# Performance work log

Hardware: AMD Instinct MI355X
Metric: run time of the kernel (lower is better)

The kernel has to match this reference:

```python
import jax, jax.numpy as jnp
import numpy as np

N = 50000          # nodes
E = 800000         # edges (before self-loops)
IN = 128           # in_channels
C = 32             # hidden_channels
H = 4              # heads
SLOPE = 0.2        # PyG GATConv default negative_slope
NUM_CLASSES = 2


def setup_inputs() -> dict:
    key = jax.random.key(0)
    ks = jax.random.split(key, 20)
    s = 0.1
    inp = {
        "x": jax.random.normal(ks[0], (N, IN), jnp.float32),
        "edge_index": jax.random.randint(ks[1], (2, E), 0, N, jnp.int64),
        # conv1: IN -> H*C (concat)
        "W1": jax.random.normal(ks[2], (IN, H * C), jnp.float32) * s,
        "a1_src": jax.random.normal(ks[3], (H, C), jnp.float32) * s,
        "a1_dst": jax.random.normal(ks[4], (H, C), jnp.float32) * s,
        "b1": jnp.zeros((H * C,), jnp.float32),
        # conv2: H*C -> H*C (concat)
        "W2": jax.random.normal(ks[5], (H * C, H * C), jnp.float32) * s,
        "a2_src": jax.random.normal(ks[6], (H, C), jnp.float32) * s,
        "a2_dst": jax.random.normal(ks[7], (H, C), jnp.float32) * s,
        "b2": jnp.zeros((H * C,), jnp.float32),
        # conv3: H*C -> C (heads=1, concat=False)
        "W3": jax.random.normal(ks[8], (H * C, C), jnp.float32) * s,
        "a3_src": jax.random.normal(ks[9], (1, C), jnp.float32) * s,
        "a3_dst": jax.random.normal(ks[10], (1, C), jnp.float32) * s,
        "b3": jnp.zeros((C,), jnp.float32),
        # node classification head: C -> 2
        "Wc": jax.random.normal(ks[11], (C, NUM_CLASSES), jnp.float32) * s,
        "bc": jnp.zeros((NUM_CLASSES,), jnp.float32),
    }
    return inp


def gat_conv(x, src, dst, W, a_src, a_dst, b, heads, out_c, concat):
    """PyG-style GATConv with self-loops already appended to (src, dst)."""
    n = x.shape[0]
    h = (x @ W).reshape(n, heads, out_c)            # [N,H,C]
    al_src = jnp.sum(h * a_src, axis=-1)            # [N,H]
    al_dst = jnp.sum(h * a_dst, axis=-1)            # [N,H]
    e = al_src[src] + al_dst[dst]                   # [Et,H]
    e = jax.nn.leaky_relu(e, SLOPE)
    # numerically-stable segment softmax over edges sharing a destination
    emax = jax.ops.segment_max(e, dst, num_segments=n)   # every node has a self-loop
    e = jnp.exp(e - emax[dst])
    denom = jax.ops.segment_sum(e, dst, num_segments=n)
    alpha = e / (denom[dst] + 1e-16)                # [Et,H]
    msg = h[src] * alpha[:, :, None]                # [Et,H,C]
    out = jax.ops.segment_sum(msg, dst, num_segments=n)  # [N,H,C]
    out = out.reshape(n, heads * out_c) if concat else jnp.mean(out, axis=1)
    return out + b


def reference(x, edge_index, W1, a1_src, a1_dst, b1, W2, a2_src, a2_dst, b2,
              W3, a3_src, a3_dst, b3, Wc, bc):
    n = x.shape[0]
    loop = jnp.arange(n, dtype=edge_index.dtype)
    src = jnp.concatenate([edge_index[0], loop])
    dst = jnp.concatenate([edge_index[1], loop])
    h = jax.nn.elu(gat_conv(x, src, dst, W1, a1_src, a1_dst, b1, H, C, True))
    h = jax.nn.elu(gat_conv(h, src, dst, W2, a2_src, a2_dst, b2, H, C, True))
    h = gat_conv(h, src, dst, W3, a3_src, a3_dst, b3, 1, C, False)
    node_output = h @ Wc + bc                       # [N,2]
    link_embedding = h                              # [N,C]
    return (node_output, link_embedding)
```

## Files before the change

### kernel.cpp

```cpp
#include <hip/hip_runtime.h>
#include <math.h>

#define SLOPE 0.2f

__device__ __forceinline__ float lrelu(float x) { return x > 0.f ? x : SLOPE * x; }

__device__ __forceinline__ float bflo(unsigned int u) { return __uint_as_float(u << 16); }
__device__ __forceinline__ float bfhi(unsigned int u) { return __uint_as_float(u & 0xffff0000u); }
__device__ __forceinline__ unsigned short f2bf(float f) {
    unsigned int u = __float_as_uint(f);
    unsigned int r = u + 0x7fffu + ((u >> 16) & 1u);
    return (unsigned short)(r >> 16);
}

template <int COUT, int Hh, int NPT>
__global__ __launch_bounds__(256) void transform_kernel(
    const float* __restrict__ xin, const float* __restrict__ W,
    const float* __restrict__ a_src, const float* __restrict__ a_dst,
    unsigned short* __restrict__ hout, float* __restrict__ alsrc,
    float* __restrict__ aldst, int N)
{
    constexpr int JT = COUT / 4;
    constexpr int GROUPS = 256 / JT;
    constexpr int NB = GROUPS * NPT;
    constexpr int PAD = 4;
    __shared__ __align__(16) float xs[NB][128 + PAD];

    const int node0 = blockIdx.x * NB;
    const int total4 = NB * 32;
    const int lim4 = (N - node0) * 32;
    const float4* src4 = (const float4*)(xin + (size_t)node0 * 128);
    for (int i = threadIdx.x; i < total4; i += 256) {
        int row = i >> 5, col = i & 31;
        float4 v = (i < lim4) ? src4[i] : make_float4(0.f, 0.f, 0.f, 0.f);
        *(float4*)&xs[row][col << 2] = v;
    }
    __syncthreads();

    const int jt = threadIdx.x % JT;
    const int g  = threadIdx.x / JT;
    const int j4 = jt * 4;

    float4 acc[NPT];
#pragma unroll
    for (int m = 0; m < NPT; ++m) acc[m] = make_float4(0.f, 0.f, 0.f, 0.f);

    const float4* Wf4 = (const float4*)W;
    for (int k4 = 0; k4 < 32; ++k4) {
        float4 w0 = Wf4[(4 * k4 + 0) * JT + jt];
        float4 w1 = Wf4[(4 * k4 + 1) * JT + jt];
        float4 w2 = Wf4[(4 * k4 + 2) * JT + jt];
        float4 w3 = Wf4[(4 * k4 + 3) * JT + jt];
#pragma unroll
        for (int m = 0; m < NPT; ++m) {
            float4 xv = *(const float4*)&xs[g * NPT + m][k4 << 2];
            acc[m].x += xv.x * w0.x + xv.y * w1.x + xv.z * w2.x + xv.w * w3.x;
            acc[m].y += xv.x * w0.y + xv.y * w1.y + xv.z * w2.y + xv.w * w3.y;
            acc[m].z += xv.x * w0.z + xv.y * w1.z + xv.z * w2.z + xv.w * w3.z;
            acc[m].w += xv.x * w0.w + xv.y * w1.w + xv.z * w2.w + xv.w * w3.w;
        }
    }

    const float4 as4 = ((const float4*)a_src)[jt];
    const float4 ad4 = ((const float4*)a_dst)[jt];
    const int hh = j4 >> 5;

#pragma unroll
    for (int m = 0; m < NPT; ++m) {
        int n = node0 + g * NPT + m;
        float4 v = acc[m];
        float sv = v.x * as4.x + v.y * as4.y + v.z * as4.z + v.w * as4.w;
        float dv = v.x * ad4.x + v.y * ad4.y + v.z * ad4.z + v.w * ad4.w;
#pragma unroll
        for (int off = 4; off >= 1; off >>= 1) {
            sv += __shfl_xor(sv, off);
            dv += __shfl_xor(dv, off);
        }
        if (n < N) {
            ushort4 hp;
            hp.x = f2bf(v.x); hp.y = f2bf(v.y);
            hp.z = f2bf(v.z); hp.w = f2bf(v.w);
            ((ushort4*)(hout + (size_t)n * COUT))[jt] = hp;
            if ((jt & 7) == 0) {
                alsrc[n * Hh + hh] = sv;
                aldst[n * Hh + hh] = dv;
            }
        }
    }
}

#define BKT_CAP 2048
#define NBKT_MAX 1024
#define CH_BIN 4096

__global__ __launch_bounds__(1024) void bin_kernel(
    const int* __restrict__ src, const int* __restrict__ dst,
    int* __restrict__ bcnt, unsigned int* __restrict__ tmp, int E, int nbkt)
{
    __shared__ int hist[NBKT_MAX];
    __shared__ int base[NBKT_MAX];
    const int e0 = blockIdx.x * CH_BIN;
    const int e1 = min(e0 + CH_BIN, E);

    for (int b = threadIdx.x; b < nbkt; b += 1024) hist[b] = 0;
    __syncthreads();
    for (int e = e0 + threadIdx.x; e < e1; e += 1024) {
        int d = __builtin_nontemporal_load(dst + e);
        atomicAdd(&hist[d >> 6], 1);
    }
    __syncthreads();
    for (int b = threadIdx.x; b < nbkt; b += 1024) {
        int c = hist[b];
        base[b] = (c > 0) ? atomicAdd(&bcnt[b << 4], c) : 0;
        hist[b] = 0;
    }
    __syncthreads();
    for (int e = e0 + threadIdx.x; e < e1; e += 1024) {
        int d = __builtin_nontemporal_load(dst + e);
        int s = __builtin_nontemporal_load(src + e);
        int b = d >> 6;
        int pos = base[b] + atomicAdd(&hist[b], 1);
        if (pos < BKT_CAP)
            tmp[((size_t)b << 11) + pos] =
                ((unsigned int)s << 6) | (unsigned int)(d & 63);
    }
}

__global__ __launch_bounds__(256) void hist_kernel(
    const unsigned int* __restrict__ tmp, const int* __restrict__ bcnt,
    int* __restrict__ deg, int N)
{
    int b = blockIdx.x;
    __shared__ int hist[64];
    if (threadIdx.x < 64) hist[threadIdx.x] = 0;
    __syncthreads();
    int cnt = min(bcnt[b << 4], BKT_CAP);
    const unsigned int* tb = tmp + ((size_t)b << 11);
    for (int i = threadIdx.x; i < cnt; i += 256)
        atomicAdd(&hist[tb[i] & 63u], 1);
    __syncthreads();
    if (threadIdx.x < 64) {
        int node = (b << 6) + threadIdx.x;
        if (node < N) deg[node] = hist[threadIdx.x];
    }
}

__global__ __launch_bounds__(256) void block_sum_kernel(
    const int* __restrict__ deg, int* __restrict__ blocksums, int N)
{
    int base = blockIdx.x * 4096 + threadIdx.x * 16;
    int s = 0;
#pragma unroll
    for (int i = 0; i < 16; ++i) {
        int idx = base + i;
        if (idx < N) s += deg[idx];
    }
#pragma unroll
    for (int off = 1; off < 64; off <<= 1) s += __shfl_xor(s, off);
    __shared__ int wsum[4];
    if ((threadIdx.x & 63) == 0) wsum[threadIdx.x >> 6] = s;
    __syncthreads();
    if (threadIdx.x == 0)
        blocksums[blockIdx.x] = wsum[0] + wsum[1] + wsum[2] + wsum[3];
}

__global__ __launch_bounds__(64) void scan_sums_kernel(
    const int* __restrict__ blocksums, int* __restrict__ blockbase,
    int* __restrict__ total_out, int nb)
{
    int tid = threadIdx.x;
    int orig = (tid < nb) ? blocksums[tid] : 0;
    int v = orig;
#pragma unroll
    for (int off = 1; off < 64; off <<= 1) {
        int t = __shfl_up(v, off);
        if (tid >= off) v += t;
    }
    if (tid < nb) blockbase[tid] = v - orig;
    if (tid == nb - 1) *total_out = v;
}

__global__ __launch_bounds__(256) void scan_final_kernel(
    const int* __restrict__ deg, const int* __restrict__ blockbase,
    int* __restrict__ offsets, int N)
{
    int base = blockIdx.x * 4096 + threadIdx.x * 16;
    int v[16];
    int s = 0;
#pragma unroll
    for (int i = 0; i < 16; ++i) {
        int idx = base + i;
        v[i] = (idx < N) ? deg[idx] : 0;
        s += v[i];
    }
    int lane = threadIdx.x & 63, wid = threadIdx.x >> 6;
    int incl = s;
#pragma unroll
    for (int off = 1; off < 64; off <<= 1) {
        int t = __shfl_up(incl, off);
        if (lane >= off) incl += t;
    }
    __shared__ int wsum[4];
    if (lane == 63) wsum[wid] = incl;
    __syncthreads();
    int woff = 0;
    for (int i = 0; i < wid; ++i) woff += wsum[i];
    int run = blockbase[blockIdx.x] + woff + incl - s;
#pragma unroll
    for (int i = 0; i < 16; ++i) {
        int idx = base + i;
        if (idx < N) offsets[idx] = run;
        run += v[i];
    }
}

__global__ __launch_bounds__(256) void place_kernel(
    const unsigned int* __restrict__ tmp, const int* __restrict__ bcnt,
    const int* __restrict__ offsets, int* __restrict__ src_sorted, int N)
{
    int b = blockIdx.x;
    __shared__ int cur[64];
    if (threadIdx.x < 64) {
        int node = (b << 6) + threadIdx.x;
        cur[threadIdx.x] = (node < N) ? offsets[node] : 0;
    }
    __syncthreads();
    int cnt = min(bcnt[b << 4], BKT_CAP);
    const unsigned int* tb = tmp + ((size_t)b << 11);
    for (int i = threadIdx.x; i < cnt; i += 256) {
        unsigned int p = tb[i];
        int pos = atomicAdd(&cur[p & 63u], 1);
        src_sorted[pos] = (int)(p >> 6);
    }
}

__device__ __forceinline__ void fma8(const uint4& p, float w, float* a) {
    a[0] += w * bflo(p.x); a[1] += w * bfhi(p.x);
    a[2] += w * bflo(p.y); a[3] += w * bfhi(p.y);
    a[4] += w * bflo(p.z); a[5] += w * bfhi(p.z);
    a[6] += w * bflo(p.w); a[7] += w * bfhi(p.w);
}

template <int Hh, int Cc, bool DO_ELU>
__global__ __launch_bounds__(256) void gat_agg_kernel(
    const int* __restrict__ offsets, const int* __restrict__ src_sorted,
    const unsigned short* __restrict__ h, const float* __restrict__ alsrc,
    const float* __restrict__ aldst, const float* __restrict__ bias,
    float* __restrict__ outf, int N)
{
    constexpr int HC  = Hh * Cc;
    constexpr int TPN = HC / 8;
    constexpr int NPB = 256 / TPN;
    constexpr int CHUNK = 64;
    __shared__ int   s_src[NPB][CHUNK];
    __shared__ __align__(16) float s_w[NPB][CHUNK][Hh];
    __shared__ int   s_nch[NPB];

    const int g  = threadIdx.x / TPN;
    const int lt = threadIdx.x % TPN;
    const int n  = blockIdx.x * NPB + g;
    const bool valid = n < N;

    int off0 = 0, deg = 0;
    if (valid) { off0 = offsets[n]; deg = offsets[n + 1] - off0; }
    if (lt == 0) s_nch[g] = (deg + CHUNK - 1) / CHUNK;
    __syncthreads();
    int maxch = 0;
#pragma unroll
    for (int i = 0; i < NPB; ++i) maxch = max(maxch, s_nch[i]);

    const int hh = (lt * 8) / Cc;
    float adv[Hh];
    if (valid) {
        if constexpr (Hh == 4) {
            float4 t = ((const float4*)aldst)[n];
            adv[0] = t.x; adv[1] = t.y; adv[2] = t.z; adv[3] = t.w;
        } else {
            adv[0] = aldst[n];
        }
    }

    const uint4* h4 = (const uint4*)h;

    float a[8] = {0.f, 0.f, 0.f, 0.f, 0.f, 0.f, 0.f, 0.f};
    float den = 0.f;
    for (int ch = 0; ch < maxch; ++ch) {
        int base = ch * CHUNK;
        int cnt = deg - base;
        cnt = cnt < 0 ? 0 : (cnt > CHUNK ? CHUNK : cnt);
        __syncthreads();
        for (int i = lt; i < cnt; i += TPN) {
            int s = src_sorted[off0 + base + i];
            s_src[g][i] = s;
            if constexpr (Hh == 4) {
                float4 av = ((const float4*)alsrc)[s];
                ((float4*)&s_w[g][i][0])[0] = make_float4(
                    __expf(lrelu(av.x + adv[0])), __expf(lrelu(av.y + adv[1])),
                    __expf(lrelu(av.z + adv[2])), __expf(lrelu(av.w + adv[3])));
            } else {
                s_w[g][i][0] = __expf(lrelu(alsrc[s] + adv[0]));
            }
        }
        __syncthreads();
        int i = 0;
        for (; i + 1 < cnt; i += 2) {
            int s0 = s_src[g][i], s1 = s_src[g][i + 1];
            float w0 = s_w[g][i][hh], w1 = s_w[g][i + 1][hh];
            uint4 p0 = h4[(size_t)s0 * TPN + lt];
            uint4 p1 = h4[(size_t)s1 * TPN + lt];
            fma8(p0, w0, a);
            fma8(p1, w1, a);
            den += w0 + w1;
        }
        if (i < cnt) {
            int s0 = s_src[g][i];
            float w0 = s_w[g][i][hh];
            uint4 p0 = h4[(size_t)s0 * TPN + lt];
            fma8(p0, w0, a);
            den += w0;
        }
    }

    if (valid) {
        float wself = __expf(lrelu(alsrc[n * Hh + hh] + adv[hh]));
        uint4 p = h4[(size_t)n * TPN + lt];
        fma8(p, wself, a);
        den += wself + 1e-16f;
        float inv = 1.f / den;
        float4 bv0 = ((const float4*)bias)[lt * 2];
        float4 bv1 = ((const float4*)bias)[lt * 2 + 1];
        float o[8];
        o[0] = a[0] * inv + bv0.x; o[1] = a[1] * inv + bv0.y;
        o[2] = a[2] * inv + bv0.z; o[3] = a[3] * inv + bv0.w;
        o[4] = a[4] * inv + bv1.x; o[5] = a[5] * inv + bv1.y;
        o[6] = a[6] * inv + bv1.z; o[7] = a[7] * inv + bv1.w;
        if (DO_ELU) {
#pragma unroll
            for (int q = 0; q < 8; ++q)
                o[q] = o[q] > 0.f ? o[q] : __expf(o[q]) - 1.f;
        }
        float4* op = (float4*)(outf + (size_t)n * HC);
        op[lt * 2]     = make_float4(o[0], o[1], o[2], o[3]);
        op[lt * 2 + 1] = make_float4(o[4], o[5], o[6], o[7]);
    }
}

__global__ __launch_bounds__(256) void head_kernel(
    const float* __restrict__ h3, const float* __restrict__ Wc,
    const float* __restrict__ bc, float* __restrict__ out, int N)
{
    int t = blockIdx.x * 256 + threadIdx.x;
    int n = t / 2, k = t % 2;
    if (n >= N) return;
    float s = bc[k];
#pragma unroll
    for (int c = 0; c < 32; ++c) s += h3[(size_t)n * 32 + c] * Wc[c * 2 + k];
    out[(size_t)n * 2 + k] = s;
}

extern "C" void kernel_launch(void* const* d_in, const int* in_sizes, int n_in,
                              void* d_out, int out_size, void* d_ws, size_t ws_size,
                              hipStream_t stream)
{
    const float* x   = (const float*)d_in[0];
    const int*   ei  = (const int*)d_in[1];
    const float* W1  = (const float*)d_in[2];
    const float* a1s = (const float*)d_in[3];
    const float* a1d = (const float*)d_in[4];
    const float* b1  = (const float*)d_in[5];
    const float* W2  = (const float*)d_in[6];
    const float* a2s = (const float*)d_in[7];
    const float* a2d = (const float*)d_in[8];
    const float* b2  = (const float*)d_in[9];
    const float* W3  = (const float*)d_in[10];
    const float* a3s = (const float*)d_in[11];
    const float* a3d = (const float*)d_in[12];
    const float* b3  = (const float*)d_in[13];
    const float* Wc  = (const float*)d_in[14];
    const float* bc  = (const float*)d_in[15];

    const int N = in_sizes[0] / 128;
    const int E = in_sizes[1] / 2;
    const int* srcIdx = ei;
    const int* dstIdx = ei + E;

    const int NBKT = (N + 63) >> 6;

    float* ws    = (float*)d_ws;
    float* fbuf  = ws;
    float* alsrc = fbuf + (size_t)N * 128;
    float* aldst = alsrc + (size_t)N * 4;
    unsigned short* hbuf = (unsigned short*)(aldst + (size_t)N * 4);
    int* deg        = (int*)(hbuf + (size_t)N * 128);
    int* offsets    = deg + N;
    int* src_sorted = offsets + N + 1;
    int* blocksums  = src_sorted + E;
    int* blockbase  = blocksums + 64;
    int* bcnt       = blockbase + 64;
    unsigned int* tmp = (unsigned int*)(bcnt + (size_t)NBKT * 16);

    float* node_out = (float*)d_out;
    float* link_out = node_out + (size_t)N * 2;

    const int nb = (N + 4095) / 4096;
    const int nbBin = (E + CH_BIN - 1) / CH_BIN;

    hipMemsetAsync(bcnt, 0, (size_t)NBKT * 16 * sizeof(int), stream);
    bin_kernel<<<nbBin, 1024, 0, stream>>>(srcIdx, dstIdx, bcnt, tmp, E, NBKT);
    hist_kernel<<<NBKT, 256, 0, stream>>>(tmp, bcnt, deg, N);
    block_sum_kernel<<<nb, 256, 0, stream>>>(deg, blocksums, N);
    scan_sums_kernel<<<1, 64, 0, stream>>>(blocksums, blockbase, offsets + N, nb);
    scan_final_kernel<<<nb, 256, 0, stream>>>(deg, blockbase, offsets, N);
    place_kernel<<<NBKT, 256, 0, stream>>>(tmp, bcnt, offsets, src_sorted, N);

    transform_kernel<128, 4, 4><<<(N + 31) / 32, 256, 0, stream>>>(
        x, W1, a1s, a1d, hbuf, alsrc, aldst, N);
    gat_agg_kernel<4, 32, true><<<(N + 15) / 16, 256, 0, stream>>>(
        offsets, src_sorted, hbuf, alsrc, aldst, b1, fbuf, N);

    transform_kernel<128, 4, 4><<<(N + 31) / 32, 256, 0, stream>>>(
        fbuf, W2, a2s, a2d, hbuf, alsrc, aldst, N);
    gat_agg_kernel<4, 32, true><<<(N + 15) / 16, 256, 0, stream>>>(
        offsets, src_sorted, hbuf, alsrc, aldst, b2, fbuf, N);

    transform_kernel<32, 1, 4><<<(N + 127) / 128, 256, 0, stream>>>(
        fbuf, W3, a3s, a3d, hbuf, alsrc, aldst, N);
    gat_agg_kernel<1, 32, false><<<(N + 63) / 64, 256, 0, stream>>>(
        offsets, src_sorted, hbuf, alsrc, aldst, b3, link_out, N);

    head_kernel<<<(N * 2 + 255) / 256, 256, 0, stream>>>(link_out, Wc, bc, node_out, N);
}
```

Baseline: 324.5 us.

## Stage weight panels through double-buffered LDS in transform kernel

```diff
diff --git a/kernel.cpp b/kernel.cpp
--- a/kernel.cpp
+++ b/kernel.cpp
@@ -24,7 +24,11 @@
     constexpr int GROUPS = 256 / JT;
     constexpr int NB = GROUPS * NPT;
     constexpr int PAD = 4;
+    constexpr int PANEL = 32;
+    constexpr int NPAN = 128 / PANEL;
+    constexpr int WL4 = PANEL * COUT / 1024;
     __shared__ __align__(16) float xs[NB][128 + PAD];
+    __shared__ __align__(16) float wls[2][PANEL][COUT];
 
     const int node0 = blockIdx.x * NB;
     const int total4 = NB * 32;
@@ -35,6 +39,17 @@
         float4 v = (i < lim4) ? src4[i] : make_float4(0.f, 0.f, 0.f, 0.f);
         *(float4*)&xs[row][col << 2] = v;
     }
+
+    const float4* W4 = (const float4*)W;
+    constexpr int P4 = PANEL * COUT / 4;
+    {
+        float4 t[WL4];
+#pragma unroll
+        for (int r = 0; r < WL4; ++r) t[r] = W4[threadIdx.x + r * 256];
+#pragma unroll
+        for (int r = 0; r < WL4; ++r)
+            ((float4*)wls[0])[threadIdx.x + r * 256] = t[r];
+    }
     __syncthreads();
 
     const int jt = threadIdx.x % JT;
@@ -45,20 +60,35 @@
 #pragma unroll
     for (int m = 0; m < NPT; ++m) acc[m] = make_float4(0.f, 0.f, 0.f, 0.f);
 
-    const float4* Wf4 = (const float4*)W;
-    for (int k4 = 0; k4 < 32; ++k4) {
-        float4 w0 = Wf4[(4 * k4 + 0) * JT + jt];
-        float4 w1 = Wf4[(4 * k4 + 1) * JT + jt];
-        float4 w2 = Wf4[(4 * k4 + 2) * JT + jt];
-        float4 w3 = Wf4[(4 * k4 + 3) * JT + jt];
-#pragma unroll
-        for (int m = 0; m < NPT; ++m) {
-            float4 xv = *(const float4*)&xs[g * NPT + m][k4 << 2];
-            acc[m].x += xv.x * w0.x + xv.y * w1.x + xv.z * w2.x + xv.w * w3.x;
-            acc[m].y += xv.x * w0.y + xv.y * w1.y + xv.z * w2.y + xv.w * w3.y;
-            acc[m].z += xv.x * w0.z + xv.y * w1.z + xv.z * w2.z + xv.w * w3.z;
-            acc[m].w += xv.x * w0.w + xv.y * w1.w + xv.z * w2.w + xv.w * w3.w;
-        }
+    for (int p = 0; p < NPAN; ++p) {
+        float4 pf[WL4];
+        if (p + 1 < NPAN) {
+#pragma unroll
+            for (int r = 0; r < WL4; ++r)
+                pf[r] = W4[(p + 1) * P4 + threadIdx.x + r * 256];
+        }
+        const int buf = p & 1;
+#pragma unroll
+        for (int k4 = 0; k4 < PANEL / 4; ++k4) {
+            float4 w0 = *(const float4*)&wls[buf][4 * k4 + 0][j4];
+            float4 w1 = *(const float4*)&wls[buf][4 * k4 + 1][j4];
+            float4 w2 = *(const float4*)&wls[buf][4 * k4 + 2][j4];
+            float4 w3 = *(const float4*)&wls[buf][4 * k4 + 3][j4];
+#pragma unroll
+            for (int m = 0; m < NPT; ++m) {
+                float4 xv = *(const float4*)&xs[g * NPT + m][p * PANEL + (k4 << 2)];
+                acc[m].x += xv.x * w0.x + xv.y * w1.x + xv.z * w2.x + xv.w * w3.x;
+                acc[m].y += xv.x * w0.y + xv.y * w1.y + xv.z * w2.y + xv.w * w3.y;
+                acc[m].z += xv.x * w0.z + xv.y * w1.z + xv.z * w2.z + xv.w * w3.z;
+                acc[m].w += xv.x * w0.w + xv.y * w1.w + xv.z * w2.w + xv.w * w3.w;
+            }
+        }
+        if (p + 1 < NPAN) {
+#pragma unroll
+            for (int r = 0; r < WL4; ++r)
+                ((float4*)wls[buf ^ 1])[threadIdx.x + r * 256] = pf[r];
+        }
+        __syncthreads();
     }
 
     const float4 as4 = ((const float4*)a_src)[jt];
```

Result: slower. 373.4 us (+15.1%).

## Use bf16 MFMA for the 128x128 GAT layer transforms

Applied to the files above, without the earlier changes.

```diff
diff --git a/kernel.cpp b/kernel.cpp
--- a/kernel.cpp
+++ b/kernel.cpp
@@ -11,6 +11,126 @@
     unsigned int u = __float_as_uint(f);
     unsigned int r = u + 0x7fffu + ((u >> 16) & 1u);
     return (unsigned short)(r >> 16);
+}
+
+typedef short frag8 __attribute__((ext_vector_type(8)));
+typedef float f32x4 __attribute__((ext_vector_type(4)));
+
+__global__ __launch_bounds__(256) void wtrans_kernel(
+    const float* __restrict__ W1, const float* __restrict__ W2,
+    unsigned short* __restrict__ Wt1, unsigned short* __restrict__ Wt2)
+{
+    int idx = blockIdx.x * 256 + threadIdx.x;
+    const float* W = W1;
+    unsigned short* Wt = Wt1;
+    int i = idx;
+    if (idx >= 16384) { W = W2; Wt = Wt2; i = idx - 16384; }
+    int n = i >> 7, k = i & 127;
+    Wt[i] = f2bf(W[k * 128 + n]);
+}
+
+__global__ __launch_bounds__(256) void transform_mfma_kernel(
+    const float* __restrict__ xin, const unsigned short* __restrict__ Wt,
+    const float* __restrict__ a_src, const float* __restrict__ a_dst,
+    unsigned short* __restrict__ hout, float* __restrict__ alsrc,
+    float* __restrict__ aldst, int N)
+{
+    constexpr int MB = 64;
+    constexpr int LDK = 136;
+    __shared__ __align__(16) unsigned short xs[MB * LDK];
+    __shared__ __align__(16) unsigned short wt[128 * LDK];
+
+    const int node0 = blockIdx.x * MB;
+    const int t = threadIdx.x;
+
+    for (int i = t; i < MB * 32; i += 256) {
+        int row = i >> 5, col4 = i & 31;
+        ushort4 o;
+        if (node0 + row < N) {
+            float4 v = ((const float4*)(xin + (size_t)(node0 + row) * 128))[col4];
+            o.x = f2bf(v.x); o.y = f2bf(v.y); o.z = f2bf(v.z); o.w = f2bf(v.w);
+        } else {
+            o.x = o.y = o.z = o.w = 0;
+        }
+        *(ushort4*)&xs[row * LDK + col4 * 4] = o;
+    }
+    for (int i = t; i < 2048; i += 256) {
+        int n = i >> 4, k16 = i & 15;
+        uint4 v = ((const uint4*)Wt)[i];
+        *(uint4*)&wt[n * LDK + k16 * 8] = v;
+    }
+    __syncthreads();
+
+    const int w    = t >> 6;
+    const int lane = t & 63;
+    const int r    = lane & 15;
+    const int q    = lane >> 4;
+
+    f32x4 acc[4][2];
+#pragma unroll
+    for (int mt = 0; mt < 4; ++mt)
+#pragma unroll
+        for (int nl = 0; nl < 2; ++nl)
+            acc[mt][nl] = (f32x4){0.f, 0.f, 0.f, 0.f};
+
+#pragma unroll
+    for (int kk = 0; kk < 4; ++kk) {
+        const int kof = kk * 32 + q * 8;
+        frag8 b0 = *(const frag8*)&wt[(w * 32 + r) * LDK + kof];
+        frag8 b1 = *(const frag8*)&wt[(w * 32 + 16 + r) * LDK + kof];
+#pragma unroll
+        for (int mt = 0; mt < 4; ++mt) {
+            frag8 a = *(const frag8*)&xs[(mt * 16 + r) * LDK + kof];
+            acc[mt][0] = __builtin_amdgcn_mfma_f32_16x16x32_bf16(a, b0, acc[mt][0], 0, 0, 0);
+            acc[mt][1] = __builtin_amdgcn_mfma_f32_16x16x32_bf16(a, b1, acc[mt][1], 0, 0, 0);
+        }
+    }
+
+    const float as0 = a_src[w * 32 + r],      ad0 = a_dst[w * 32 + r];
+    const float as1 = a_src[w * 32 + 16 + r], ad1 = a_dst[w * 32 + 16 + r];
+#pragma unroll
+    for (int mt = 0; mt < 4; ++mt) {
+#pragma unroll
+        for (int reg = 0; reg < 4; ++reg) {
+            float s = acc[mt][0][reg] * as0 + acc[mt][1][reg] * as1;
+            float d = acc[mt][0][reg] * ad0 + acc[mt][1][reg] * ad1;
+#pragma unroll
+            for (int off = 1; off < 16; off <<= 1) {
+                s += __shfl_xor(s, off);
+                d += __shfl_xor(d, off);
+            }
+            if (r == 0) {
+                int m = mt * 16 + q * 4 + reg;
+                int n = node0 + m;
+                if (n < N) {
+                    alsrc[n * 4 + w] = s;
+                    aldst[n * 4 + w] = d;
+                }
+            }
+        }
+    }
+
+    __syncthreads();
+#pragma unroll
+    for (int mt = 0; mt < 4; ++mt)
+#pragma unroll
+        for (int nl = 0; nl < 2; ++nl)
+#pragma unroll
+            for (int reg = 0; reg < 4; ++reg) {
+                int m = mt * 16 + q * 4 + reg;
+                int n = w * 32 + nl * 16 + r;
+                xs[m * LDK + n] = f2bf(acc[mt][nl][reg]);
+            }
+    __syncthreads();
+    {
+        int row = t >> 2, cbase = (t & 3) * 32;
+        if (node0 + row < N) {
+            uint4* dst = (uint4*)(hout + (size_t)(node0 + row) * 128 + cbase);
+#pragma unroll
+            for (int j = 0; j < 4; ++j)
+                dst[j] = *(const uint4*)&xs[row * LDK + cbase + j * 8];
+        }
+    }
 }
 
 template <int COUT, int Hh, int NPT>
@@ -396,7 +516,10 @@
     int* src_sorted = offsets + N + 1;
     int* blocksums  = src_sorted + E;
     int* blockbase  = blocksums + 64;
-    int* bcnt       = blockbase + 64;
+    uintptr_t wp = ((uintptr_t)(blockbase + 64) + 15) & ~(uintptr_t)15;
+    unsigned short* wt1 = (unsigned short*)wp;
+    unsigned short* wt2 = wt1 + 16384;
+    int* bcnt       = (int*)(wt2 + 16384);
     unsigned int* tmp = (unsigned int*)(bcnt + (size_t)NBKT * 16);
 
     float* node_out = (float*)d_out;
@@ -405,6 +528,7 @@
     const int nb = (N + 4095) / 4096;
     const int nbBin = (E + CH_BIN - 1) / CH_BIN;
 
+    wtrans_kernel<<<128, 256, 0, stream>>>(W1, W2, wt1, wt2);
     hipMemsetAsync(bcnt, 0, (size_t)NBKT * 16 * sizeof(int), stream);
     bin_kernel<<<nbBin, 1024, 0, stream>>>(srcIdx, dstIdx, bcnt, tmp, E, NBKT);
     hist_kernel<<<NBKT, 256, 0, stream>>>(tmp, bcnt, deg, N);
@@ -413,13 +537,13 @@
     scan_final_kernel<<<nb, 256, 0, stream>>>(deg, blockbase, offsets, N);
     place_kernel<<<NBKT, 256, 0, stream>>>(tmp, bcnt, offsets, src_sorted, N);
 
-    transform_kernel<128, 4, 4><<<(N + 31) / 32, 256, 0, stream>>>(
-        x, W1, a1s, a1d, hbuf, alsrc, aldst, N);
+    transform_mfma_kernel<<<(N + 63) / 64, 256, 0, stream>>>(
+        x, wt1, a1s, a1d, hbuf, alsrc, aldst, N);
     gat_agg_kernel<4, 32, true><<<(N + 15) / 16, 256, 0, stream>>>(
         offsets, src_sorted, hbuf, alsrc, aldst, b1, fbuf, N);
 
-    transform_kernel<128, 4, 4><<<(N + 31) / 32, 256, 0, stream>>>(
-        fbuf, W2, a2s, a2d, hbuf, alsrc, aldst, N);
+    transform_mfma_kernel<<<(N + 63) / 64, 256, 0, stream>>>(
+        fbuf, wt2, a2s, a2d, hbuf, alsrc, aldst, N);
     gat_agg_kernel<4, 32, true><<<(N + 15) / 16, 256, 0, stream>>>(
         offsets, src_sorted, hbuf, alsrc, aldst, b2, fbuf, N);
 
```

Result: faster. 295.5 us (-8.9%).
